# Kernel optimization log

Measured on AMD Instinct MI355X. Metric: run time of the kernel, lower is better.

## Reference

```python
import jax, jax.numpy as jnp
import numpy as np

N_NODES = 100000
N_EDGES = 3200000
N_REL = 16
EMB = 32
N_CLS = 50
BATCH = 1024


def setup_inputs() -> dict:
    key = jax.random.key(0)
    ks = jax.random.split(key, 8)
    return {
        "emb0": jax.random.normal(ks[0], (N_NODES, EMB), dtype=jnp.float32),
        "W1": jax.random.normal(ks[1], (N_REL, EMB, EMB), dtype=jnp.float32),
        "W2": jax.random.normal(ks[2], (N_REL, EMB, EMB), dtype=jnp.float32),
        "cls_w": jax.random.normal(ks[3], (N_CLS, EMB), dtype=jnp.float32),
        "cls_b": jax.random.normal(ks[4], (N_CLS,), dtype=jnp.float32),
        "src": jax.random.randint(ks[5], (N_EDGES,), 0, N_NODES, dtype=jnp.int64) if jax.config.jax_enable_x64 else jax.random.randint(ks[5], (N_EDGES,), 0, N_NODES).astype(jnp.int64),
        "rel": jax.random.randint(ks[6], (N_EDGES,), 0, N_REL).astype(jnp.int64),
        "dst": jax.random.randint(ks[7], (N_EDGES,), 0, N_NODES).astype(jnp.int64),
        "b": BATCH,
    }


def reference(emb0, W1, W2, cls_w, cls_b, src, rel, dst, b):
    n, e = emb0.shape
    r = W1.shape[0]
    # fr = src + n * rel : row index of the (r*n, n) sparse adjacency, per SimpleRGCN
    fr = (src + n * rel).astype(jnp.int32)
    dst_i = dst.astype(jnp.int32)
    # util.sum_sparse: normalize each edge by the sum over its row (out-degree per (rel, src))
    deg = jax.ops.segment_sum(jnp.ones((fr.shape[0],), dtype=emb0.dtype), fr, num_segments=r * n)
    vals = 1.0 / deg[fr]  # [E]; only evaluated at rows with >=1 edge

    def rgcn_layer(h, W):
        # util.spmm: output[fr] += vals * h[dst]  -> (r*n, e)
        msgs = vals[:, None] * h[dst_i]                       # [E, e]
        agg = jax.ops.segment_sum(msgs, fr, num_segments=r * n)
        agg = agg.reshape(r, n, e)                            # [r, n, e]
        # einsum('rij, rnj -> nri').sum(dim=1) == einsum('rij, rnj -> ni')
        return jax.nn.relu(jnp.einsum('rij,rnj->ni', W, agg))

    h = rgcn_layer(emb0, W1)
    h = rgcn_layer(h, W2)
    pooled = h[:b]                                            # batch entities occupy first b slots
    return pooled @ cls_w.T + cls_b
```

## Files before the change

kernel.cpp:

```cpp
#include <hip/hip_runtime.h>
#include <stdint.h>

#define N_NODES 100000
#define N_EDGES 3200000
#define N_REL   16
#define NBKT    391
#define NBLK    256
#define EPB     12500
#define BKT_PAD 1800
#define PADDED_E (N_EDGES + 8 + NBKT * BKT_PAD)
#define PAD_FLAG 0x80000000u

typedef __attribute__((ext_vector_type(8))) short  short8;
typedef __attribute__((ext_vector_type(4))) short  short4_t;
typedef __attribute__((ext_vector_type(4))) float  f32x4;

static __device__ __forceinline__ int align8(int x) { return (x + 7) & ~7; }

static __device__ __forceinline__ unsigned short f32_to_bf16(float f) {
    union { float f; unsigned int u; } v; v.f = f;
    unsigned int u = v.u;
    unsigned int r = u + 0x7FFFu + ((u >> 16) & 1u);
    return (unsigned short)(r >> 16);
}
static __device__ __forceinline__ float bf2f(unsigned short s) {
    union { unsigned int u; float f; } cv; cv.u = ((unsigned int)s) << 16;
    return cv.f;
}

__global__ __launch_bounds__(512) void k_histA(const int* __restrict__ src,
                                               int* __restrict__ table) {
    __shared__ int lh[NBKT];
    int tid = threadIdx.x, bid = blockIdx.x;
    for (int t = tid; t < NBKT; t += 512) lh[t] = 0;
    __syncthreads();
    int e0 = bid * EPB;
    for (int e = e0 + tid; e < e0 + EPB; e += 512)
        atomicAdd(&lh[src[e] >> 8], 1);
    __syncthreads();
    for (int t = tid; t < NBKT; t += 512) table[bid * NBKT + t] = lh[t];
}

__global__ void k_btot(const int* __restrict__ table, int* __restrict__ btot) {
    int b = blockIdx.x * 256 + threadIdx.x;
    if (b >= NBKT) return;
    int s = 0;
    for (int k = 0; k < NBLK; ++k) s += table[k * NBKT + b];
    btot[b] = s;
}

__global__ void k_bbase(const int* __restrict__ btot, int* __restrict__ bktbase) {
    __shared__ int sd[512];
    int tid = threadIdx.x;
    int v = (tid < NBKT) ? btot[tid] : 0;
    sd[tid] = v; __syncthreads();
    int x = v;
    for (int off = 1; off < 512; off <<= 1) {
        int t = (tid >= off) ? sd[tid - off] : 0;
        __syncthreads();
        x += t; sd[tid] = x;
        __syncthreads();
    }
    if (tid < NBKT) bktbase[tid] = x - v;
    if (tid == 0) bktbase[NBKT] = N_EDGES;
}

__global__ void k_goff(const int* __restrict__ table, const int* __restrict__ bktbase,
                       int* __restrict__ goff) {
    __shared__ int sd[NBLK];
    int b = blockIdx.x;
    int tid = threadIdx.x;
    int v = table[tid * NBKT + b];
    sd[tid] = v; __syncthreads();
    int x = v;
    for (int off = 1; off < NBLK; off <<= 1) {
        int t = (tid >= off) ? sd[tid - off] : 0;
        __syncthreads();
        x += t; sd[tid] = x;
        __syncthreads();
    }
    int bp = align8(bktbase[b]) + b * BKT_PAD;
    goff[tid * NBKT + b] = bp + (x - v);
}

__global__ __launch_bounds__(512) void k_partB(const int* __restrict__ src,
                                               const int* __restrict__ rel,
                                               const int* __restrict__ dst,
                                               const int* __restrict__ goff,
                                               unsigned int* __restrict__ part) {
    __shared__ int lcur[NBKT];
    int tid = threadIdx.x, bid = blockIdx.x;
    for (int t = tid; t < NBKT; t += 512) lcur[t] = goff[bid * NBKT + t];
    __syncthreads();
    int e0 = bid * EPB;
    for (int e = e0 + tid; e < e0 + EPB; e += 512) {
        int s = src[e];
        int pos = atomicAdd(&lcur[s >> 8], 1);
        part[pos] = ((unsigned)(s & 255) << 21) | ((unsigned)rel[e] << 17) | (unsigned)dst[e];
    }
}

__global__ __launch_bounds__(256) void k_place(const unsigned int* __restrict__ part,
                                               const int* __restrict__ bktbase,
                                               unsigned int* __restrict__ sorted_rd,
                                               int* __restrict__ sorted_src,
                                               int* __restrict__ offs,
                                               int* __restrict__ cnt,
                                               float* __restrict__ inv2) {
    __shared__ int lhist[256 * 16];
    __shared__ int sd[256];
    __shared__ int lcur[256];
    int b = blockIdx.x, tid = threadIdx.x;
    int n0 = b << 8;
    int braw = bktbase[b];
    int bsize = bktbase[b + 1] - braw;
    int bp = align8(braw) + b * BKT_PAD;
    int bp_next = align8(bktbase[b + 1]) + (b + 1) * BKT_PAD;
#pragma unroll
    for (int k = 0; k < 16; ++k) lhist[tid + k * 256] = 0;
    __syncthreads();
    for (int t = bp + tid; t < bp + bsize; t += 256)
        atomicAdd(&lhist[part[t] >> 17], 1);
    __syncthreads();
    int ncnt = 0;
#pragma unroll
    for (int r = 0; r < 16; ++r) ncnt += lhist[(tid << 4) | r];
    int ncnt_p = align8(ncnt);
    sd[tid] = ncnt_p; __syncthreads();
    int x = ncnt_p;
    for (int off = 1; off < 256; off <<= 1) {
        int t = (tid >= off) ? sd[tid - off] : 0;
        __syncthreads();
        x += t; sd[tid] = x;
        __syncthreads();
    }
    int nodeoff = bp + (x - ncnt_p);
    lcur[tid] = nodeoff;
    int node = n0 + tid;
    if (node < N_NODES) { offs[node] = nodeoff; cnt[node] = ncnt; }
    for (int t = tid; t < 4096; t += 256) {
        int nd = n0 + (t >> 4);
        if (nd < N_NODES) {
            int c = lhist[t];
            inv2[((size_t)nd << 4) + (t & 15)] = c ? 1.0f / (float)c : 0.f;
        }
    }
    __syncthreads();
    for (int t = bp + tid; t < bp + bsize; t += 256) {
        unsigned int v = part[t];
        int j = (int)(v >> 21);
        int p = atomicAdd(&lcur[j], 1);
        sorted_rd[p] = v & 0x1FFFFFu;
        if (b < 4) sorted_src[p] = n0 + j;
    }
    __syncthreads();
    for (int p = nodeoff + ncnt; p < nodeoff + ncnt_p; ++p) sorted_rd[p] = PAD_FLAG;
    int content_end = bp + sd[255];
    for (int t = content_end + tid; t < bp_next; t += 256) sorted_rd[t] = PAD_FLAG;
}

__global__ __launch_bounds__(256) void k_pgemm(const float* __restrict__ emb0,
                                               const float* __restrict__ W1,
                                               unsigned short* __restrict__ P,
                                               int nwaves) {
    __shared__ unsigned short wlds[512 * 32];
    int tid = threadIdx.x;
    for (int t = tid; t < 4096; t += 256) {
        f32x4 v = ((const f32x4*)W1)[t];
        short4_t o;
#pragma unroll
        for (int e = 0; e < 4; ++e) o[e] = (short)f32_to_bf16(v[e]);
        ((short4_t*)wlds)[t] = o;
    }
    __syncthreads();

    int gw   = (blockIdx.x * 256 + tid) >> 6;
    int lane = tid & 63;
    int col16 = lane & 15, krow = lane >> 4;

    const int NTILES = N_NODES / 16;
    for (int tile = gw; tile < NTILES; tile += nwaves) {
        int n0 = tile * 16;
        const float* ap = emb0 + (size_t)(n0 + col16) * 32 + krow * 8;
        f32x4 a0 = *(const f32x4*)ap;
        f32x4 a1 = *(const f32x4*)(ap + 4);
        short8 b;
#pragma unroll
        for (int e = 0; e < 4; ++e) { b[e] = (short)f32_to_bf16(a0[e]); b[e + 4] = (short)f32_to_bf16(a1[e]); }
#pragma unroll
        for (int rcb = 0; rcb < 32; ++rcb) {
            short8 a = *(const short8*)&wlds[(size_t)(rcb * 16 + col16) * 32 + krow * 8];
            f32x4 c = {0.f, 0.f, 0.f, 0.f};
            c = __builtin_amdgcn_mfma_f32_16x16x32_bf16(a, b, c, 0, 0, 0);
            short4_t o;
#pragma unroll
            for (int reg = 0; reg < 4; ++reg) o[reg] = (short)f32_to_bf16(c[reg]);
            *(short4_t*)(P + (size_t)(n0 + col16) * 512 + rcb * 16 + krow * 4) = o;
        }
    }
}

__global__ __launch_bounds__(256) void k_agg1(const unsigned int* __restrict__ sorted_rd,
                                              const int* __restrict__ offs,
                                              const int* __restrict__ cnt,
                                              const float* __restrict__ inv2,
                                              const unsigned short* __restrict__ P,
                                              float* __restrict__ h1) {
    int node = blockIdx.x * 4 + (threadIdx.x >> 6);
    int lane = threadIdx.x & 63;
    int i = lane & 31, h = lane >> 5;
    int start = offs[node];
    int ecp = align8(cnt[node]);
    const float* ivn = inv2 + ((size_t)node << 4);
    float acc = 0.f;
    for (int t0 = start + h * 8; t0 < start + ecp; t0 += 16) {
        uint4 qa = *reinterpret_cast<const uint4*>(sorted_rd + t0);
        uint4 qb = *reinterpret_cast<const uint4*>(sorted_rd + t0 + 4);
        unsigned pk[8] = {qa.x, qa.y, qa.z, qa.w, qb.x, qb.y, qb.z, qb.w};
        float v[8], val[8];
#pragma unroll
        for (int k = 0; k < 8; ++k) {
            unsigned d = pk[k] & 0x1FFFFu, r = (pk[k] >> 17) & 15u;
            v[k]   = bf2f(P[(size_t)d * 512 + r * 32 + i]);
            val[k] = (pk[k] & PAD_FLAG) ? 0.f : ivn[r];
        }
#pragma unroll
        for (int k = 0; k < 8; ++k) acc += val[k] * v[k];
    }
    acc += __shfl_xor(acc, 32, 64);
    if (h == 0) h1[(size_t)node * 32 + i] = fmaxf(acc, 0.f);
}

__global__ void k_agg2(const unsigned int* __restrict__ sorted_rd,
                       const int* __restrict__ sorted_src,
                       const int* __restrict__ bktbase,
                       const float* __restrict__ inv2, const float* __restrict__ h1,
                       float* __restrict__ agg2) {
    int E2 = ((bktbase[4] + 7) & ~7) + 4 * BKT_PAD;
    long total = (long)E2 * 32;
    long stride = (long)gridDim.x * blockDim.x;
    for (long t = (long)blockIdx.x * blockDim.x + threadIdx.x; t < total; t += stride) {
        int e = (int)(t >> 5), j = (int)(t & 31);
        unsigned int pk = sorted_rd[e];
        if (pk & PAD_FLAG) continue;
        int r = (int)(pk >> 17), d = (int)(pk & 0x1FFFFu);
        int s = sorted_src[e];
        float val = inv2[((size_t)s << 4) + r];
        atomicAdd(&agg2[(s << 9) + (r << 5) + j], val * h1[(size_t)d * 32 + j]);
    }
}

__global__ void k_h2(const float* __restrict__ agg2, const float* __restrict__ W2,
                     float* __restrict__ h2pre) {
    int t = blockIdx.x * 256 + threadIdx.x;
    int s = t >> 5, i = t & 31;
    const float* arow = agg2 + (s << 9);
    float acc = 0.f;
#pragma unroll 4
    for (int r = 0; r < 16; ++r) {
        const float* wrow = W2 + r * 1024 + i * 32;
        const float* a = arow + r * 32;
#pragma unroll
        for (int j = 0; j < 32; ++j) acc += wrow[j] * a[j];
    }
    h2pre[t] = acc;
}

__global__ void k_cls(const float* __restrict__ h2pre, const float* __restrict__ cls_w,
                      const float* __restrict__ cls_b, float* __restrict__ out) {
    int t = blockIdx.x * 256 + threadIdx.x;
    int b = t >> 6, c = t & 63;
    if (b >= 1024 || c >= 50) return;
    float acc = cls_b[c];
#pragma unroll
    for (int j = 0; j < 32; ++j)
        acc += fmaxf(h2pre[b * 32 + j], 0.f) * cls_w[c * 32 + j];
    out[b * 50 + c] = acc;
}

extern "C" void kernel_launch(void* const* d_in, const int* in_sizes, int n_in,
                              void* d_out, int out_size, void* d_ws, size_t ws_size,
                              hipStream_t stream) {
    const float* emb0  = (const float*)d_in[0];
    const float* W1    = (const float*)d_in[1];
    const float* W2    = (const float*)d_in[2];
    const float* cls_w = (const float*)d_in[3];
    const float* cls_b = (const float*)d_in[4];
    const int*   src   = (const int*)d_in[5];
    const int*   rel   = (const int*)d_in[6];
    const int*   dst   = (const int*)d_in[7];
    float* out = (float*)d_out;

    char* ws = (char*)d_ws;
    size_t off = 0;
    auto alloc = [&](size_t bytes) -> void* {
        void* p = ws + off;
        off = (off + bytes + 255) & ~((size_t)255);
        return p;
    };
    float*          inv2       = (float*)alloc((size_t)N_NODES * 16 * 4);
    int*            offs       = (int*)alloc((size_t)N_NODES * 4);
    int*            cnt        = (int*)alloc((size_t)N_NODES * 4);
    int*            table      = (int*)alloc((size_t)NBLK * NBKT * 4);
    int*            btot       = (int*)alloc((size_t)NBKT * 4);
    int*            bktbase    = (int*)alloc((size_t)(NBKT + 1) * 4);
    int*            goff       = (int*)alloc((size_t)NBLK * NBKT * 4);
    unsigned int*   sorted_rd  = (unsigned int*)alloc((size_t)PADDED_E * 4);
    int*            sorted_src = (int*)alloc((size_t)PADDED_E * 4);
    unsigned short* P          = (unsigned short*)alloc((size_t)N_NODES * 512 * 2);
    float*          h1         = (float*)alloc((size_t)N_NODES * 32 * 4);
    float*          agg2       = (float*)alloc((size_t)1024 * 512 * 4);
    float*          h2pre      = (float*)alloc((size_t)1024 * 32 * 4);
    unsigned int*   part       = (unsigned int*)P;

    hipMemsetAsync(agg2, 0, (size_t)1024 * 512 * 4, stream);

    k_histA <<<NBLK, 512, 0, stream>>>(src, table);
    k_btot  <<<2, 256, 0, stream>>>(table, btot);
    k_bbase <<<1, 512, 0, stream>>>(btot, bktbase);
    k_goff  <<<NBKT, NBLK, 0, stream>>>(table, bktbase, goff);
    k_partB <<<NBLK, 512, 0, stream>>>(src, rel, dst, goff, part);
    k_place <<<NBKT, 256, 0, stream>>>(part, bktbase, sorted_rd, sorted_src, offs, cnt, inv2);
    k_pgemm <<<391, 256, 0, stream>>>(emb0, W1, P, 391 * 4);
    k_agg1  <<<25000, 256, 0, stream>>>(sorted_rd, offs, cnt, inv2, P, h1);
    k_agg2  <<<1024, 256, 0, stream>>>(sorted_rd, sorted_src, bktbase, inv2, h1, agg2);
    k_h2    <<<128, 256, 0, stream>>>(agg2, W2, h2pre);
    k_cls   <<<256, 256, 0, stream>>>(h2pre, cls_w, cls_b, out);
}
```

Before: 352.7 us.

## Fuse edge partition with projection GEMM and widen agg1 edge chunks to 16

Merges the edge partition kernel and the per-relation projection GEMM into one launch with heterogeneous blocks. The partition buffer moves out of P into its own workspace, so the scatter and the GEMM can run concurrently instead of back-to-back. Per-node padding goes from 8 to 16 edges so agg1 can load 16 packed edges per half-wave, giving more gathers in flight. h1 now aliases the partition buffer and sorted_src shrinks. The cost is more padding work for low-degree nodes and larger LDS use in the fused kernel.

```diff
diff --git a/kernel.cpp b/kernel.cpp
--- a/kernel.cpp
+++ b/kernel.cpp
@@ -7,15 +7,16 @@
 #define NBKT    391
 #define NBLK    256
 #define EPB     12500
-#define BKT_PAD 1800
-#define PADDED_E (N_EDGES + 8 + NBKT * BKT_PAD)
+#define NPGB    200
+#define BKT_PAD 3856
+#define PADDED_E (N_EDGES + 16 + NBKT * BKT_PAD)
 #define PAD_FLAG 0x80000000u
 
 typedef __attribute__((ext_vector_type(8))) short  short8;
 typedef __attribute__((ext_vector_type(4))) short  short4_t;
 typedef __attribute__((ext_vector_type(4))) float  f32x4;
 
-static __device__ __forceinline__ int align8(int x) { return (x + 7) & ~7; }
+static __device__ __forceinline__ int align16i(int x) { return (x + 15) & ~15; }
 
 static __device__ __forceinline__ unsigned short f32_to_bf16(float f) {
     union { float f; unsigned int u; } v; v.f = f;
@@ -79,24 +80,63 @@
         x += t; sd[tid] = x;
         __syncthreads();
     }
-    int bp = align8(bktbase[b]) + b * BKT_PAD;
+    int bp = align16i(bktbase[b]) + b * BKT_PAD;
     goff[tid * NBKT + b] = bp + (x - v);
 }
 
-__global__ __launch_bounds__(512) void k_partB(const int* __restrict__ src,
-                                               const int* __restrict__ rel,
-                                               const int* __restrict__ dst,
-                                               const int* __restrict__ goff,
-                                               unsigned int* __restrict__ part) {
+__global__ __launch_bounds__(512) void k_partB_pgemm(const int* __restrict__ src,
+                                                     const int* __restrict__ rel,
+                                                     const int* __restrict__ dst,
+                                                     const int* __restrict__ goff,
+                                                     unsigned int* __restrict__ part,
+                                                     const float* __restrict__ emb0,
+                                                     const float* __restrict__ W1,
+                                                     unsigned short* __restrict__ P) {
     __shared__ int lcur[NBKT];
+    __shared__ unsigned short wlds[512 * 32];
     int tid = threadIdx.x, bid = blockIdx.x;
-    for (int t = tid; t < NBKT; t += 512) lcur[t] = goff[bid * NBKT + t];
-    __syncthreads();
-    int e0 = bid * EPB;
-    for (int e = e0 + tid; e < e0 + EPB; e += 512) {
-        int s = src[e];
-        int pos = atomicAdd(&lcur[s >> 8], 1);
-        part[pos] = ((unsigned)(s & 255) << 21) | ((unsigned)rel[e] << 17) | (unsigned)dst[e];
+    if (bid < NBLK) {
+        for (int t = tid; t < NBKT; t += 512) lcur[t] = goff[bid * NBKT + t];
+        __syncthreads();
+        int e0 = bid * EPB;
+        for (int e = e0 + tid; e < e0 + EPB; e += 512) {
+            int s = src[e];
+            int pos = atomicAdd(&lcur[s >> 8], 1);
+            part[pos] = ((unsigned)(s & 255) << 21) | ((unsigned)rel[e] << 17) | (unsigned)dst[e];
+        }
+    } else {
+        int pb = bid - NBLK;
+        for (int t = tid; t < 4096; t += 512) {
+            f32x4 v = ((const f32x4*)W1)[t];
+            short4_t o;
+#pragma unroll
+            for (int e = 0; e < 4; ++e) o[e] = (short)f32_to_bf16(v[e]);
+            ((short4_t*)wlds)[t] = o;
+        }
+        __syncthreads();
+        int gw   = pb * 8 + (tid >> 6);
+        int lane = tid & 63;
+        int col16 = lane & 15, krow = lane >> 4;
+        const int NTILES = N_NODES / 16;
+        for (int tile = gw; tile < NTILES; tile += NPGB * 8) {
+            int n0 = tile * 16;
+            const float* ap = emb0 + (size_t)(n0 + col16) * 32 + krow * 8;
+            f32x4 a0 = *(const f32x4*)ap;
+            f32x4 a1 = *(const f32x4*)(ap + 4);
+            short8 b;
+#pragma unroll
+            for (int e = 0; e < 4; ++e) { b[e] = (short)f32_to_bf16(a0[e]); b[e + 4] = (short)f32_to_bf16(a1[e]); }
+#pragma unroll
+            for (int rcb = 0; rcb < 32; ++rcb) {
+                short8 a = *(const short8*)&wlds[(size_t)(rcb * 16 + col16) * 32 + krow * 8];
+                f32x4 c = {0.f, 0.f, 0.f, 0.f};
+                c = __builtin_amdgcn_mfma_f32_16x16x32_bf16(a, b, c, 0, 0, 0);
+                short4_t o;
+#pragma unroll
+                for (int reg = 0; reg < 4; ++reg) o[reg] = (short)f32_to_bf16(c[reg]);
+                *(short4_t*)(P + (size_t)(n0 + col16) * 512 + rcb * 16 + krow * 4) = o;
+            }
+        }
     }
 }
 
@@ -114,8 +154,8 @@
     int n0 = b << 8;
     int braw = bktbase[b];
     int bsize = bktbase[b + 1] - braw;
-    int bp = align8(braw) + b * BKT_PAD;
-    int bp_next = align8(bktbase[b + 1]) + (b + 1) * BKT_PAD;
+    int bp = align16i(braw) + b * BKT_PAD;
+    int bp_next = align16i(bktbase[b + 1]) + (b + 1) * BKT_PAD;
 #pragma unroll
     for (int k = 0; k < 16; ++k) lhist[tid + k * 256] = 0;
     __syncthreads();
@@ -125,7 +165,7 @@
     int ncnt = 0;
 #pragma unroll
     for (int r = 0; r < 16; ++r) ncnt += lhist[(tid << 4) | r];
-    int ncnt_p = align8(ncnt);
+    int ncnt_p = align16i(ncnt);
     sd[tid] = ncnt_p; __syncthreads();
     int x = ncnt_p;
     for (int off = 1; off < 256; off <<= 1) {
@@ -157,47 +197,6 @@
     for (int p = nodeoff + ncnt; p < nodeoff + ncnt_p; ++p) sorted_rd[p] = PAD_FLAG;
     int content_end = bp + sd[255];
     for (int t = content_end + tid; t < bp_next; t += 256) sorted_rd[t] = PAD_FLAG;
-}
-
-__global__ __launch_bounds__(256) void k_pgemm(const float* __restrict__ emb0,
-                                               const float* __restrict__ W1,
-                                               unsigned short* __restrict__ P,
-                                               int nwaves) {
-    __shared__ unsigned short wlds[512 * 32];
-    int tid = threadIdx.x;
-    for (int t = tid; t < 4096; t += 256) {
-        f32x4 v = ((const f32x4*)W1)[t];
-        short4_t o;
-#pragma unroll
-        for (int e = 0; e < 4; ++e) o[e] = (short)f32_to_bf16(v[e]);
-        ((short4_t*)wlds)[t] = o;
-    }
-    __syncthreads();
-
-    int gw   = (blockIdx.x * 256 + tid) >> 6;
-    int lane = tid & 63;
-    int col16 = lane & 15, krow = lane >> 4;
-
-    const int NTILES = N_NODES / 16;
-    for (int tile = gw; tile < NTILES; tile += nwaves) {
-        int n0 = tile * 16;
-        const float* ap = emb0 + (size_t)(n0 + col16) * 32 + krow * 8;
-        f32x4 a0 = *(const f32x4*)ap;
-        f32x4 a1 = *(const f32x4*)(ap + 4);
-        short8 b;
-#pragma unroll
-        for (int e = 0; e < 4; ++e) { b[e] = (short)f32_to_bf16(a0[e]); b[e + 4] = (short)f32_to_bf16(a1[e]); }
-#pragma unroll
-        for (int rcb = 0; rcb < 32; ++rcb) {
-            short8 a = *(const short8*)&wlds[(size_t)(rcb * 16 + col16) * 32 + krow * 8];
-            f32x4 c = {0.f, 0.f, 0.f, 0.f};
-            c = __builtin_amdgcn_mfma_f32_16x16x32_bf16(a, b, c, 0, 0, 0);
-            short4_t o;
-#pragma unroll
-            for (int reg = 0; reg < 4; ++reg) o[reg] = (short)f32_to_bf16(c[reg]);
-            *(short4_t*)(P + (size_t)(n0 + col16) * 512 + rcb * 16 + krow * 4) = o;
-        }
-    }
 }
 
 __global__ __launch_bounds__(256) void k_agg1(const unsigned int* __restrict__ sorted_rd,
@@ -210,22 +209,25 @@
     int lane = threadIdx.x & 63;
     int i = lane & 31, h = lane >> 5;
     int start = offs[node];
-    int ecp = align8(cnt[node]);
+    int ecp = align16i(cnt[node]);
     const float* ivn = inv2 + ((size_t)node << 4);
     float acc = 0.f;
-    for (int t0 = start + h * 8; t0 < start + ecp; t0 += 16) {
+    for (int t0 = start + h * 16; t0 < start + ecp; t0 += 32) {
         uint4 qa = *reinterpret_cast<const uint4*>(sorted_rd + t0);
         uint4 qb = *reinterpret_cast<const uint4*>(sorted_rd + t0 + 4);
-        unsigned pk[8] = {qa.x, qa.y, qa.z, qa.w, qb.x, qb.y, qb.z, qb.w};
-        float v[8], val[8];
-#pragma unroll
-        for (int k = 0; k < 8; ++k) {
+        uint4 qc = *reinterpret_cast<const uint4*>(sorted_rd + t0 + 8);
+        uint4 qd = *reinterpret_cast<const uint4*>(sorted_rd + t0 + 12);
+        unsigned pk[16] = {qa.x, qa.y, qa.z, qa.w, qb.x, qb.y, qb.z, qb.w,
+                           qc.x, qc.y, qc.z, qc.w, qd.x, qd.y, qd.z, qd.w};
+        float v[16], val[16];
+#pragma unroll
+        for (int k = 0; k < 16; ++k) {
             unsigned d = pk[k] & 0x1FFFFu, r = (pk[k] >> 17) & 15u;
             v[k]   = bf2f(P[(size_t)d * 512 + r * 32 + i]);
             val[k] = (pk[k] & PAD_FLAG) ? 0.f : ivn[r];
         }
 #pragma unroll
-        for (int k = 0; k < 8; ++k) acc += val[k] * v[k];
+        for (int k = 0; k < 16; ++k) acc += val[k] * v[k];
     }
     acc += __shfl_xor(acc, 32, 64);
     if (h == 0) h1[(size_t)node * 32 + i] = fmaxf(acc, 0.f);
@@ -236,7 +238,7 @@
                        const int* __restrict__ bktbase,
                        const float* __restrict__ inv2, const float* __restrict__ h1,
                        float* __restrict__ agg2) {
-    int E2 = ((bktbase[4] + 7) & ~7) + 4 * BKT_PAD;
+    int E2 = ((bktbase[4] + 15) & ~15) + 4 * BKT_PAD;
     long total = (long)E2 * 32;
     long stride = (long)gridDim.x * blockDim.x;
     for (long t = (long)blockIdx.x * blockDim.x + threadIdx.x; t < total; t += stride) {
@@ -306,24 +308,24 @@
     int*            bktbase    = (int*)alloc((size_t)(NBKT + 1) * 4);
     int*            goff       = (int*)alloc((size_t)NBLK * NBKT * 4);
     unsigned int*   sorted_rd  = (unsigned int*)alloc((size_t)PADDED_E * 4);
-    int*            sorted_src = (int*)alloc((size_t)PADDED_E * 4);
+    int*            sorted_src = (int*)alloc((size_t)65536 * 4);
+    unsigned int*   partX      = (unsigned int*)alloc((size_t)PADDED_E * 4);
     unsigned short* P          = (unsigned short*)alloc((size_t)N_NODES * 512 * 2);
-    float*          h1         = (float*)alloc((size_t)N_NODES * 32 * 4);
     float*          agg2       = (float*)alloc((size_t)1024 * 512 * 4);
     float*          h2pre      = (float*)alloc((size_t)1024 * 32 * 4);
-    unsigned int*   part       = (unsigned int*)P;
+    unsigned int*   part       = partX;
+    float*          h1         = (float*)partX;
 
     hipMemsetAsync(agg2, 0, (size_t)1024 * 512 * 4, stream);
 
-    k_histA <<<NBLK, 512, 0, stream>>>(src, table);
-    k_btot  <<<2, 256, 0, stream>>>(table, btot);
-    k_bbase <<<1, 512, 0, stream>>>(btot, bktbase);
-    k_goff  <<<NBKT, NBLK, 0, stream>>>(table, bktbase, goff);
-    k_partB <<<NBLK, 512, 0, stream>>>(src, rel, dst, goff, part);
-    k_place <<<NBKT, 256, 0, stream>>>(part, bktbase, sorted_rd, sorted_src, offs, cnt, inv2);
-    k_pgemm <<<391, 256, 0, stream>>>(emb0, W1, P, 391 * 4);
-    k_agg1  <<<25000, 256, 0, stream>>>(sorted_rd, offs, cnt, inv2, P, h1);
-    k_agg2  <<<1024, 256, 0, stream>>>(sorted_rd, sorted_src, bktbase, inv2, h1, agg2);
-    k_h2    <<<128, 256, 0, stream>>>(agg2, W2, h2pre);
-    k_cls   <<<256, 256, 0, stream>>>(h2pre, cls_w, cls_b, out);
-}
+    k_histA       <<<NBLK, 512, 0, stream>>>(src, table);
+    k_btot        <<<2, 256, 0, stream>>>(table, btot);
+    k_bbase       <<<1, 512, 0, stream>>>(btot, bktbase);
+    k_goff        <<<NBKT, NBLK, 0, stream>>>(table, bktbase, goff);
+    k_partB_pgemm <<<NBLK + NPGB, 512, 0, stream>>>(src, rel, dst, goff, part, emb0, W1, P);
+    k_place       <<<NBKT, 256, 0, stream>>>(part, bktbase, sorted_rd, sorted_src, offs, cnt, inv2);
+    k_agg1        <<<25000, 256, 0, stream>>>(sorted_rd, offs, cnt, inv2, P, h1);
+    k_agg2        <<<1024, 256, 0, stream>>>(sorted_rd, sorted_src, bktbase, inv2, h1, agg2);
+    k_h2          <<<128, 256, 0, stream>>>(agg2, W2, h2pre);
+    k_cls         <<<256, 256, 0, stream>>>(h2pre, cls_w, cls_b, out);
+}
```

Result: faster. 345.6 us (-2.0%).
